# Kernel optimization log

Measured on AMD Instinct MI355X. Metric: run time of the kernel, lower is better.

Reference implementation:

```python
import jax, jax.numpy as jnp
import numpy as np


def setup_inputs() -> dict:
    key = jax.random.key(0)
    k1, k2, k3 = jax.random.split(key, 3)
    B, C, D, H, W = 4, 64, 32, 64, 64
    x = jax.random.normal(k1, (B, C, D, H, W), dtype=jnp.float32)
    # Conv3d(in=2, out=1, k=7), PyTorch default init: U(-s, s), s = 1/sqrt(fan_in)
    fan_in = 2 * 7 * 7 * 7
    s = 1.0 / np.sqrt(fan_in)
    conv_w = jax.random.uniform(k2, (1, 2, 7, 7, 7), dtype=jnp.float32, minval=-s, maxval=s)
    conv_b = jax.random.uniform(k3, (1,), dtype=jnp.float32, minval=-s, maxval=s)
    return {"x": x, "conv_w": conv_w, "conv_b": conv_b}


def reference(x, conv_w, conv_b):
    # channel-wise max and mean -> [B, 2, D, H, W]
    xc = jnp.stack([jnp.max(x, axis=1), jnp.mean(x, axis=1)], axis=1)
    # conv3d 2->1, k7, stride 1, padding 3 (SAME)
    y = jax.lax.conv_general_dilated(
        xc, conv_w,
        window_strides=(1, 1, 1),
        padding=[(3, 3), (3, 3), (3, 3)],
        dimension_numbers=("NCDHW", "OIDHW", "NCDHW"),
    ) + conv_b[None, :, None, None, None]
    scale = jax.nn.sigmoid(y)  # [B, 1, D, H, W]
    return x * scale
```

## Files before the change

kernel.cpp:

```cpp
#include <hip/hip_runtime.h>
#include <math.h>

#define B_ 4
#define C_ 64
#define D_ 32
#define H_ 64
#define W_ 64
#define S_ (D_*H_*W_)
#define S4_ (S_/4)
#define HW_ (H_*W_)

typedef float floatx4 __attribute__((ext_vector_type(4)));

__global__ __launch_bounds__(256) void reduce_kernel(const float* __restrict__ x,
                                                     float* __restrict__ xc) {
    int i  = blockIdx.x * 256 + threadIdx.x;
    int b  = i >> 15;
    int s4 = i & (S4_ - 1);
    const float4* x4 = reinterpret_cast<const float4*>(x) + (size_t)b * C_ * S4_ + s4;
    float4 v = x4[0];
    float mx0 = v.x, mx1 = v.y, mx2 = v.z, mx3 = v.w;
    float sm0 = v.x, sm1 = v.y, sm2 = v.z, sm3 = v.w;
    #pragma unroll 8
    for (int c = 1; c < C_; ++c) {
        float4 t = x4[(size_t)c * S4_];
        mx0 = fmaxf(mx0, t.x); sm0 += t.x;
        mx1 = fmaxf(mx1, t.y); sm1 += t.y;
        mx2 = fmaxf(mx2, t.z); sm2 += t.z;
        mx3 = fmaxf(mx3, t.w); sm3 += t.w;
    }
    float4* o = reinterpret_cast<float4*>(xc);
    float4 a; a.x = mx0; a.y = mx1; a.z = mx2; a.w = mx3;
    o[((size_t)b * 2 + 0) * S4_ + s4] = a;
    const float inv = 1.0f / 64.0f;
    float4 m; m.x = sm0 * inv; m.y = sm1 * inv; m.z = sm2 * inv; m.w = sm3 * inv;
    o[((size_t)b * 2 + 1) * S4_ + s4] = m;
}

#define TZ 10
#define TY 14
#define TXS 72
#define PLANE (TY*TXS)
#define CHSZ (TZ*PLANE)
#define HALO_N (2*TZ*TY*70)

__global__ __launch_bounds__(256, 1) void conv_gate_kernel(const float* __restrict__ xc,
                                                           const float* __restrict__ x,
                                                           const float* __restrict__ cw,
                                                           const float* __restrict__ cb,
                                                           float* __restrict__ out) {
    __shared__ __align__(16) float tile[2 * CHSZ];
    __shared__ __align__(16) float wl[784];

    const int tid = threadIdx.x;
    const int b  = blockIdx.z >> 3;
    const int d0 = (blockIdx.z & 7) * 4;
    const int h0 = blockIdx.y * 8;

    const int w4 = tid & 15;
    const int hh = (tid >> 4) & 7;
    const int dd = tid >> 7;
    const int dbase = d0 + 2 * dd;

    for (int idx = tid; idx < 784; idx += 256) {
        int ch = idx / 392;
        int r  = idx - ch * 392;
        int kz = r / 56;
        int r2 = r - kz * 56;
        int ky = r2 >> 3;
        int kw = r2 & 7;
        wl[idx] = (kw < 7) ? cw[ch * 343 + kz * 49 + ky * 7 + kw] : 0.f;
    }

    for (int base = tid; base < HALO_N; base += 256 * 8) {
        float sv[8];
        int   sa[8];
        #pragma unroll
        for (int k = 0; k < 8; ++k) {
            int idx = base + k * 256;
            sv[k] = 0.f;
            sa[k] = -1;
            if (idx < HALO_N) {
                int ch = idx / 9800;
                int r  = idx - ch * 9800;
                int z  = r / 980;
                int r2 = r - z * 980;
                int y  = r2 / 70;
                int xw = r2 - y * 70;
                sa[k] = ch * CHSZ + z * PLANE + y * TXS + xw;
                int gd = d0 + z - 3, gh = h0 + y - 3, gw = xw - 3;
                if ((unsigned)gd < (unsigned)D_ && (unsigned)gh < (unsigned)H_ &&
                    (unsigned)gw < (unsigned)W_)
                    sv[k] = xc[(size_t)(b * 2 + ch) * S_ + gd * HW_ + gh * W_ + gw];
            }
        }
        #pragma unroll
        for (int k = 0; k < 8; ++k)
            if (sa[k] >= 0) tile[sa[k]] = sv[k];
    }
    __syncthreads();

    float acc0[4] = {0.f, 0.f, 0.f, 0.f};
    float acc1[4] = {0.f, 0.f, 0.f, 0.f};
    for (int ch = 0; ch < 2; ++ch) {
        const float* tch = &tile[ch * CHSZ + 2 * dd * PLANE + w4 * 4];
        const float* wch = &wl[ch * 392];
        for (int ky = 0; ky < 7; ++ky) {
            const float* trow = tch + (hh + ky) * TXS;
            const float* wrow = wch + ky * 8;
            float wp[7];
            #pragma unroll
            for (int z = 0; z < 8; ++z) {
                const float* rp = trow + z * PLANE;
                float4 f0 = *reinterpret_cast<const float4*>(rp);
                float4 f1 = *reinterpret_cast<const float4*>(rp + 4);
                float2 f2 = *reinterpret_cast<const float2*>(rp + 8);
                float win[10] = {f0.x, f0.y, f0.z, f0.w,
                                 f1.x, f1.y, f1.z, f1.w, f2.x, f2.y};
                if (z >= 1) {
                    #pragma unroll
                    for (int kw = 0; kw < 7; ++kw) {
                        acc1[0] = fmaf(win[kw + 0], wp[kw], acc1[0]);
                        acc1[1] = fmaf(win[kw + 1], wp[kw], acc1[1]);
                        acc1[2] = fmaf(win[kw + 2], wp[kw], acc1[2]);
                        acc1[3] = fmaf(win[kw + 3], wp[kw], acc1[3]);
                    }
                }
                if (z < 7) {
                    float4 wa = *reinterpret_cast<const float4*>(wrow + z * 56);
                    float4 wb = *reinterpret_cast<const float4*>(wrow + z * 56 + 4);
                    float wc[7] = {wa.x, wa.y, wa.z, wa.w, wb.x, wb.y, wb.z};
                    #pragma unroll
                    for (int kw = 0; kw < 7; ++kw) {
                        acc0[0] = fmaf(win[kw + 0], wc[kw], acc0[0]);
                        acc0[1] = fmaf(win[kw + 1], wc[kw], acc0[1]);
                        acc0[2] = fmaf(win[kw + 2], wc[kw], acc0[2]);
                        acc0[3] = fmaf(win[kw + 3], wc[kw], acc0[3]);
                    }
                    #pragma unroll
                    for (int k = 0; k < 7; ++k) wp[k] = wc[k];
                }
            }
        }
    }

    const float bias = cb[0];
    floatx4 s0, s1;
    s0.x = 1.0f / (1.0f + __expf(-(acc0[0] + bias)));
    s0.y = 1.0f / (1.0f + __expf(-(acc0[1] + bias)));
    s0.z = 1.0f / (1.0f + __expf(-(acc0[2] + bias)));
    s0.w = 1.0f / (1.0f + __expf(-(acc0[3] + bias)));
    s1.x = 1.0f / (1.0f + __expf(-(acc1[0] + bias)));
    s1.y = 1.0f / (1.0f + __expf(-(acc1[1] + bias)));
    s1.z = 1.0f / (1.0f + __expf(-(acc1[2] + bias)));
    s1.w = 1.0f / (1.0f + __expf(-(acc1[3] + bias)));

    const int h = h0 + hh, w = w4 * 4;
    const size_t sp = (size_t)dbase * HW_ + (size_t)h * W_ + w;
    const float* xp = x + (size_t)b * C_ * S_ + sp;
    float* op = out + (size_t)b * C_ * S_ + sp;
    for (int c = 0; c < C_; c += 8) {
        floatx4 v[16];
        #pragma unroll
        for (int k = 0; k < 8; ++k) {
            const size_t off = (size_t)(c + k) * S_;
            v[2 * k]     = *reinterpret_cast<const floatx4*>(xp + off);
            v[2 * k + 1] = *reinterpret_cast<const floatx4*>(xp + off + HW_);
        }
        #pragma unroll
        for (int k = 0; k < 8; ++k) {
            const size_t off = (size_t)(c + k) * S_;
            *reinterpret_cast<floatx4*>(op + off)       = v[2 * k] * s0;
            *reinterpret_cast<floatx4*>(op + off + HW_) = v[2 * k + 1] * s1;
        }
    }
}

extern "C" void kernel_launch(void* const* d_in, const int* in_sizes, int n_in,
                              void* d_out, int out_size, void* d_ws, size_t ws_size,
                              hipStream_t stream) {
    const float* x  = (const float*)d_in[0];
    const float* cw = (const float*)d_in[1];
    const float* cb = (const float*)d_in[2];
    float* out = (float*)d_out;
    float* xc  = (float*)d_ws;

    reduce_kernel<<<dim3((B_ * S4_) / 256), dim3(256), 0, stream>>>(x, xc);
    conv_gate_kernel<<<dim3(1, H_ / 8, B_ * (D_ / 4)), dim3(256), 0, stream>>>(
        xc, x, cw, cb, out);
}
```

Before: 90.07 us.

## Fuse channel reduction into conv-gate kernel with neighbor flag synchronization

```diff
diff --git a/kernel.cpp b/kernel.cpp
--- a/kernel.cpp
+++ b/kernel.cpp
@@ -12,31 +12,6 @@
 
 typedef float floatx4 __attribute__((ext_vector_type(4)));
 
-__global__ __launch_bounds__(256) void reduce_kernel(const float* __restrict__ x,
-                                                     float* __restrict__ xc) {
-    int i  = blockIdx.x * 256 + threadIdx.x;
-    int b  = i >> 15;
-    int s4 = i & (S4_ - 1);
-    const float4* x4 = reinterpret_cast<const float4*>(x) + (size_t)b * C_ * S4_ + s4;
-    float4 v = x4[0];
-    float mx0 = v.x, mx1 = v.y, mx2 = v.z, mx3 = v.w;
-    float sm0 = v.x, sm1 = v.y, sm2 = v.z, sm3 = v.w;
-    #pragma unroll 8
-    for (int c = 1; c < C_; ++c) {
-        float4 t = x4[(size_t)c * S4_];
-        mx0 = fmaxf(mx0, t.x); sm0 += t.x;
-        mx1 = fmaxf(mx1, t.y); sm1 += t.y;
-        mx2 = fmaxf(mx2, t.z); sm2 += t.z;
-        mx3 = fmaxf(mx3, t.w); sm3 += t.w;
-    }
-    float4* o = reinterpret_cast<float4*>(xc);
-    float4 a; a.x = mx0; a.y = mx1; a.z = mx2; a.w = mx3;
-    o[((size_t)b * 2 + 0) * S4_ + s4] = a;
-    const float inv = 1.0f / 64.0f;
-    float4 m; m.x = sm0 * inv; m.y = sm1 * inv; m.z = sm2 * inv; m.w = sm3 * inv;
-    o[((size_t)b * 2 + 1) * S4_ + s4] = m;
-}
-
 #define TZ 10
 #define TY 14
 #define TXS 72
@@ -44,23 +19,57 @@
 #define CHSZ (TZ*PLANE)
 #define HALO_N (2*TZ*TY*70)
 
-__global__ __launch_bounds__(256, 1) void conv_gate_kernel(const float* __restrict__ xc,
-                                                           const float* __restrict__ x,
-                                                           const float* __restrict__ cw,
-                                                           const float* __restrict__ cb,
-                                                           float* __restrict__ out) {
+__global__ __launch_bounds__(256, 1) void fused_kernel(const float* __restrict__ x,
+                                                       const float* __restrict__ cw,
+                                                       const float* __restrict__ cb,
+                                                       float* __restrict__ xc,
+                                                       unsigned int* __restrict__ flags,
+                                                       float* __restrict__ out) {
     __shared__ __align__(16) float tile[2 * CHSZ];
     __shared__ __align__(16) float wl[784];
 
     const int tid = threadIdx.x;
-    const int b  = blockIdx.z >> 3;
-    const int d0 = (blockIdx.z & 7) * 4;
-    const int h0 = blockIdx.y * 8;
-
-    const int w4 = tid & 15;
-    const int hh = (tid >> 4) & 7;
-    const int dd = tid >> 7;
-    const int dbase = d0 + 2 * dd;
+    const int b  = (int)blockIdx.z >> 3;
+    const int dt = (int)blockIdx.z & 7;
+    const int ht = (int)blockIdx.y;
+    const int d0 = dt * 4;
+    const int h0 = ht * 8;
+
+    {
+        const float4* xb = reinterpret_cast<const float4*>(x) + (size_t)b * C_ * S4_;
+        float4* xcmax  = reinterpret_cast<float4*>(xc) + (size_t)(b * 2 + 0) * S4_;
+        float4* xcmean = reinterpret_cast<float4*>(xc) + (size_t)(b * 2 + 1) * S4_;
+        #pragma unroll
+        for (int rep = 0; rep < 2; ++rep) {
+            int p  = tid + rep * 256;
+            int w4 = p & 15;
+            int hh = (p >> 4) & 7;
+            int dz = p >> 7;
+            int sp4 = (d0 + dz) * (HW_ / 4) + (h0 + hh) * (W_ / 4) + w4;
+            const float4* xp = xb + sp4;
+            float4 v = xp[0];
+            float mx0 = v.x, mx1 = v.y, mx2 = v.z, mx3 = v.w;
+            float sm0 = v.x, sm1 = v.y, sm2 = v.z, sm3 = v.w;
+            #pragma unroll 8
+            for (int c = 1; c < C_; ++c) {
+                float4 t = xp[(size_t)c * S4_];
+                mx0 = fmaxf(mx0, t.x); sm0 += t.x;
+                mx1 = fmaxf(mx1, t.y); sm1 += t.y;
+                mx2 = fmaxf(mx2, t.z); sm2 += t.z;
+                mx3 = fmaxf(mx3, t.w); sm3 += t.w;
+            }
+            float4 a; a.x = mx0; a.y = mx1; a.z = mx2; a.w = mx3;
+            xcmax[sp4] = a;
+            const float inv = 1.0f / 64.0f;
+            float4 m; m.x = sm0 * inv; m.y = sm1 * inv; m.z = sm2 * inv; m.w = sm3 * inv;
+            xcmean[sp4] = m;
+        }
+    }
+    __threadfence();
+    __syncthreads();
+    if (tid == 0)
+        __hip_atomic_store(&flags[(int)blockIdx.z * 8 + ht], 1u,
+                           __ATOMIC_RELEASE, __HIP_MEMORY_SCOPE_AGENT);
 
     for (int idx = tid; idx < 784; idx += 256) {
         int ch = idx / 392;
@@ -71,6 +80,19 @@
         int kw = r2 & 7;
         wl[idx] = (kw < 7) ? cw[ch * 343 + kz * 49 + ky * 7 + kw] : 0.f;
     }
+
+    if (tid < 9) {
+        int nd = dt + (tid % 3) - 1;
+        int nh = ht + (tid / 3) - 1;
+        if (nd >= 0 && nd < 8 && nh >= 0 && nh < 8) {
+            const unsigned int* f = &flags[(b * 8 + nd) * 8 + nh];
+            while (__hip_atomic_load(f, __ATOMIC_ACQUIRE,
+                                     __HIP_MEMORY_SCOPE_AGENT) == 0u)
+                __builtin_amdgcn_s_sleep(2);
+        }
+    }
+    __syncthreads();
+    __threadfence();
 
     for (int base = tid; base < HALO_N; base += 256 * 8) {
         float sv[8];
@@ -99,6 +121,11 @@
             if (sa[k] >= 0) tile[sa[k]] = sv[k];
     }
     __syncthreads();
+
+    const int w4 = tid & 15;
+    const int hh = (tid >> 4) & 7;
+    const int dd = tid >> 7;
+    const int dbase = d0 + 2 * dd;
 
     float acc0[4] = {0.f, 0.f, 0.f, 0.f};
     float acc1[4] = {0.f, 0.f, 0.f, 0.f};
@@ -184,8 +211,10 @@
     const float* cb = (const float*)d_in[2];
     float* out = (float*)d_out;
     float* xc  = (float*)d_ws;
-
-    reduce_kernel<<<dim3((B_ * S4_) / 256), dim3(256), 0, stream>>>(x, xc);
-    conv_gate_kernel<<<dim3(1, H_ / 8, B_ * (D_ / 4)), dim3(256), 0, stream>>>(
-        xc, x, cw, cb, out);
+    unsigned int* flags =
+        (unsigned int*)((char*)d_ws + (size_t)B_ * 2 * S_ * sizeof(float));
+
+    hipMemsetAsync(flags, 0, 256 * sizeof(unsigned int), stream);
+    fused_kernel<<<dim3(1, H_ / 8, B_ * (D_ / 4)), dim3(256), 0, stream>>>(
+        x, cw, cb, xc, flags, out);
 }
```

Measured after the change: 142.9 us. 58.7% more time.
